# Kernel tuning notes

Hardware: AMD Instinct MI355X
Metric: run time of the kernel (lower is better)

The kernel has to match this reference:

```python
import jax, jax.numpy as jnp
import numpy as np

PAD = 0  # padding_idx for all int feature columns


def setup_inputs() -> dict:
    key = jax.random.key(0)
    ks = jax.random.split(key, 8)
    B = 16384
    return {
        "item_hist": jax.random.randint(ks[0], (B, 50), 0, 100000, dtype=jnp.int64 if jax.config.jax_enable_x64 else jnp.int32).astype(jnp.int32),
        "cate_hist": jax.random.randint(ks[1], (B, 50), 0, 100000).astype(jnp.int32),
        "ctx_ids": jax.random.randint(ks[2], (B, 20), 0, 1000).astype(jnp.int32),
        "price": jax.random.normal(ks[3], (B, 1), dtype=jnp.float32),
        "dense_vec": jax.random.normal(ks[4], (B, 128), dtype=jnp.float32),
        "W_item": jax.random.normal(ks[5], (100000, 64), dtype=jnp.float32),
        "W_cate": jax.random.normal(ks[6], (100000, 64), dtype=jnp.float32),
        "W_ctx": jax.random.normal(ks[7], (1000, 32), dtype=jnp.float32),
    }


def reference(item_hist, cate_hist, ctx_ids, price, dense_vec, W_item, W_cate, W_ctx):
    # torch Embedding with padding_idx: row PAD is zero (and receives no grad)
    Wi = W_item.at[PAD].set(0.0)
    Wc = W_cate.at[PAD].set(0.0)
    Wx = W_ctx.at[PAD].set(0.0)
    # sum merger: [B, L, D] -> [B, D]
    e_item = jnp.take(Wi, item_hist, axis=0).sum(axis=-2)
    # mean merger (divides by L including padding slots, as torch .mean does)
    e_cate = jnp.take(Wc, cate_hist, axis=0).mean(axis=-2)
    # concat merger: [B, L, D] -> [B, L*D]
    B = ctx_ids.shape[0]
    e_ctx = jnp.take(Wx, ctx_ids, axis=0).reshape(B, -1)
    # FeatureLayer concatenates columns in declared order
    return jnp.concatenate([e_item, e_cate, e_ctx, price, dense_vec], axis=-1)
```

## Files before the change

### kernel.cpp

```cpp
#include <hip/hip_runtime.h>


#define LH 50
#define LC 20
#define DI 64
#define DC 64
#define DX 32
#define DDENSE 128
#define OUT_D 897
#define ROWS 4
#define BLK_OUT (ROWS * OUT_D)
#define NROW_TAB 100000
#define TAB_ELEMS (NROW_TAB * 64)
#define NIT8 7

typedef float    f32x4 __attribute__((ext_vector_type(4)));
typedef _Float16 f16x4 __attribute__((ext_vector_type(4)));
typedef _Float16 f16x8 __attribute__((ext_vector_type(8)));

__global__ __launch_bounds__(256) void convert_tables_kernel(
    const float* __restrict__ Wi, const float* __restrict__ Wc,
    _Float16* __restrict__ Hi, _Float16* __restrict__ Hc)
{
    const int stride = gridDim.x * blockDim.x;
    for (int i = blockIdx.x * blockDim.x + threadIdx.x;
         i < TAB_ELEMS / 4; i += stride) {
        const f32x4 a = reinterpret_cast<const f32x4*>(Wi)[i];
        const f32x4 b = reinterpret_cast<const f32x4*>(Wc)[i];
        f16x4 ha, hb;
        #pragma unroll
        for (int e = 0; e < 4; ++e) { ha[e] = (_Float16)a[e]; hb[e] = (_Float16)b[e]; }
        reinterpret_cast<f16x4*>(Hi)[i] = ha;
        reinterpret_cast<f16x4*>(Hc)[i] = hb;
    }
}

template <bool HALF>
__global__ __launch_bounds__(256) void featlayer_kernel(
    const int* __restrict__ item_hist,
    const int* __restrict__ cate_hist,
    const int* __restrict__ ctx_ids,
    const float* __restrict__ price,
    const float* __restrict__ dense_vec,
    const float* __restrict__ W_item,
    const float* __restrict__ W_cate,
    const _Float16* __restrict__ H_item,
    const _Float16* __restrict__ H_cate,
    const float* __restrict__ W_ctx,
    float* __restrict__ out,
    int B)
{
    __shared__ __align__(16) float obuf[BLK_OUT];
    __shared__ int ih_s[ROWS * LH];
    __shared__ int ch_s[ROWS * LH];
    __shared__ int cx_s[ROWS * LC];

    const int t     = threadIdx.x;
    const int rbase = blockIdx.x * ROWS;

    if (t < ROWS * LH) {
        ih_s[t] = item_hist[(size_t)rbase * LH + t];
        ch_s[t] = cate_hist[(size_t)rbase * LH + t];
    }
    if (t < ROWS * LC) cx_s[t] = ctx_ids[(size_t)rbase * LC + t];

    if (t < 128) {
        const int r = t >> 5;
        const int c = t & 31;
        const f32x4 dvv = *reinterpret_cast<const f32x4*>(
            dense_vec + ((size_t)(rbase + r) * DDENSE + c * 4));
        float* o = obuf + r * OUT_D + (DI + DC + LC * DX + 1) + c * 4;
        o[0] = dvv.x; o[1] = dvv.y; o[2] = dvv.z; o[3] = dvv.w;
    }
    if (t < ROWS) obuf[t * OUT_D + DI + DC + LC * DX] = price[rbase + t];

    __syncthreads();

    const int w    = t >> 6;
    const int lane = t & 63;

    if (HALF) {
        const int sub8 = lane >> 3;
        const int l8   = lane & 7;

        int idxI[NIT8], idxC[NIT8];
        #pragma unroll
        for (int k = 0; k < NIT8; ++k) {
            const int ki = sub8 + 8 * k;
            idxI[k] = (ki < LH) ? ih_s[w * LH + ki] : 0;
            idxC[k] = (ki < LH) ? ch_s[w * LH + ki] : 0;
        }

        float iacc[8] = {0,0,0,0,0,0,0,0};
        float cacc[8] = {0,0,0,0,0,0,0,0};
        #pragma unroll
        for (int k = 0; k < NIT8; ++k) {
            const f16x8 vi = *reinterpret_cast<const f16x8*>(
                H_item + ((size_t)idxI[k] * 64 + l8 * 8));
            const f16x8 vc = *reinterpret_cast<const f16x8*>(
                H_cate + ((size_t)idxC[k] * 64 + l8 * 8));
            const float si = (idxI[k] != 0) ? 1.0f : 0.0f;
            const float sc = (idxC[k] != 0) ? 1.0f : 0.0f;
            #pragma unroll
            for (int e = 0; e < 8; ++e) {
                iacc[e] += (float)vi[e] * si;
                cacc[e] += (float)vc[e] * sc;
            }
        }

        #pragma unroll
        for (int e = 0; e < 8; ++e) {
            float a = iacc[e];
            a += __shfl_xor(a, 8, 64);
            a += __shfl_xor(a, 16, 64);
            a += __shfl_xor(a, 32, 64);
            iacc[e] = a;
            float c = cacc[e];
            c += __shfl_xor(c, 8, 64);
            c += __shfl_xor(c, 16, 64);
            c += __shfl_xor(c, 32, 64);
            cacc[e] = c;
        }

        if (sub8 == 0) {
            float* oi = obuf + w * OUT_D + l8 * 8;
            float* oc = obuf + w * OUT_D + DI + l8 * 8;
            const float inv = 1.0f / (float)LH;
            #pragma unroll
            for (int e = 0; e < 8; ++e) {
                oi[e] = iacc[e];
                oc[e] = cacc[e] * inv;
            }
        }
    } else {
        const int sub = lane >> 4;
        const int l16 = lane & 15;
        int idxI[13], idxC[13];
        #pragma unroll
        for (int k = 0; k < 13; ++k) {
            const int ki = sub + 4 * k;
            idxI[k] = (ki < LH) ? ih_s[w * LH + ki] : 0;
            idxC[k] = (ki < LH) ? ch_s[w * LH + ki] : 0;
        }
        f32x4 iacc = {0,0,0,0}, cacc = {0,0,0,0};
        #pragma unroll
        for (int k = 0; k < 13; ++k) {
            const f32x4 vi = *reinterpret_cast<const f32x4*>(
                W_item + ((size_t)idxI[k] * DI + l16 * 4));
            const f32x4 vc = *reinterpret_cast<const f32x4*>(
                W_cate + ((size_t)idxC[k] * DC + l16 * 4));
            iacc += vi * ((idxI[k] != 0) ? 1.0f : 0.0f);
            cacc += vc * ((idxC[k] != 0) ? 1.0f : 0.0f);
        }
        #pragma unroll
        for (int e = 0; e < 4; ++e) {
            float a = iacc[e];
            a += __shfl_xor(a, 16, 64); a += __shfl_xor(a, 32, 64);
            iacc[e] = a;
            float c = cacc[e];
            c += __shfl_xor(c, 16, 64); c += __shfl_xor(c, 32, 64);
            cacc[e] = c;
        }
        if (sub == 0) {
            float* oi = obuf + w * OUT_D + l16 * 4;
            float* oc = obuf + w * OUT_D + DI + l16 * 4;
            const float inv = 1.0f / (float)LH;
            #pragma unroll
            for (int e = 0; e < 4; ++e) { oi[e] = iacc[e]; oc[e] = cacc[e] * inv; }
        }
    }

    #pragma unroll
    for (int t2 = 0; t2 < 3; ++t2) {
        const int c = lane + 64 * t2;
        if (c < (LC * DX) / 4) {
            const int id = cx_s[w * LC + (c >> 3)];
            f32x4 v = {0.f, 0.f, 0.f, 0.f};
            if (id != 0)
                v = *reinterpret_cast<const f32x4*>(
                    W_ctx + ((size_t)id * DX + (c & 7) * 4));
            float* o = obuf + w * OUT_D + DI + DC + 4 * c;
            o[0] = v.x; o[1] = v.y; o[2] = v.z; o[3] = v.w;
        }
    }

    __syncthreads();

    float* __restrict__ oblk = out + (size_t)rbase * OUT_D;
    #pragma unroll
    for (int i = 0; i < 4; ++i) {
        const int c = t + 256 * i;
        if (c < BLK_OUT / 4) {
            const f32x4 v = *reinterpret_cast<const f32x4*>(obuf + 4 * c);
            *reinterpret_cast<f32x4*>(oblk + 4 * c) = v;
        }
    }
}

extern "C" void kernel_launch(void* const* d_in, const int* in_sizes, int n_in,
                              void* d_out, int out_size, void* d_ws, size_t ws_size,
                              hipStream_t stream) {
    const int*   item_hist = (const int*)  d_in[0];
    const int*   cate_hist = (const int*)  d_in[1];
    const int*   ctx_ids   = (const int*)  d_in[2];
    const float* price     = (const float*)d_in[3];
    const float* dense_vec = (const float*)d_in[4];
    const float* W_item    = (const float*)d_in[5];
    const float* W_cate    = (const float*)d_in[6];
    const float* W_ctx     = (const float*)d_in[7];
    float* out = (float*)d_out;

    const int B = in_sizes[0] / LH;
    const int grid = (B + ROWS - 1) / ROWS;

    const size_t tab_bytes = (size_t)TAB_ELEMS * sizeof(_Float16);
    if (ws_size >= 2 * tab_bytes) {
        _Float16* Hi = (_Float16*)d_ws;
        _Float16* Hc = Hi + TAB_ELEMS;
        convert_tables_kernel<<<2048, 256, 0, stream>>>(W_item, W_cate, Hi, Hc);
        featlayer_kernel<true><<<grid, 256, 0, stream>>>(
            item_hist, cate_hist, ctx_ids, price, dense_vec,
            W_item, W_cate, Hi, Hc, W_ctx, out, B);
    } else {
        featlayer_kernel<false><<<grid, 256, 0, stream>>>(
            item_hist, cate_hist, ctx_ids, price, dense_vec,
            W_item, W_cate, nullptr, nullptr, W_ctx, out, B);
    }
}
```

Baseline: 58.36 us.

## Quantize embedding tables to int8 with per-row scales and ctx table to fp16

Replaces the fp16 conversion of the item and category tables with int8 quantization using a per-row absmax scale, and also converts the ctx table to fp16. The gather kernel reads 16 bytes of int8 per lane and dequantizes with the row scale, and the ctx gather reads fp16. This halves conversion writes and gather traffic, at the cost of much larger numerical error from 8-bit quantization.

```diff
diff --git a/kernel.cpp b/kernel.cpp
--- a/kernel.cpp
+++ b/kernel.cpp
@@ -12,30 +12,65 @@
 #define BLK_OUT (ROWS * OUT_D)
 #define NROW_TAB 100000
 #define TAB_ELEMS (NROW_TAB * 64)
-#define NIT8 7
 
 typedef float    f32x4 __attribute__((ext_vector_type(4)));
+typedef int      i32x4 __attribute__((ext_vector_type(4)));
 typedef _Float16 f16x4 __attribute__((ext_vector_type(4)));
 typedef _Float16 f16x8 __attribute__((ext_vector_type(8)));
 
-__global__ __launch_bounds__(256) void convert_tables_kernel(
+#define QI_OFF  0
+#define QC_OFF  6400000
+#define SCI_OFF 12800000
+#define SCC_OFF 13200000
+#define HX_OFF  13600000
+#define WS_NEED 13664000
+#define CONV_TAB_BLOCKS 12500
+#define CTX_CHUNKS 8000
+
+__global__ __launch_bounds__(256) void convert_kernel(
     const float* __restrict__ Wi, const float* __restrict__ Wc,
-    _Float16* __restrict__ Hi, _Float16* __restrict__ Hc)
+    const float* __restrict__ Wx,
+    signed char* __restrict__ Qi, signed char* __restrict__ Qc,
+    float* __restrict__ ScI, float* __restrict__ ScC,
+    _Float16* __restrict__ Hx)
 {
-    const int stride = gridDim.x * blockDim.x;
-    for (int i = blockIdx.x * blockDim.x + threadIdx.x;
-         i < TAB_ELEMS / 4; i += stride) {
-        const f32x4 a = reinterpret_cast<const f32x4*>(Wi)[i];
-        const f32x4 b = reinterpret_cast<const f32x4*>(Wc)[i];
-        f16x4 ha, hb;
-        #pragma unroll
-        for (int e = 0; e < 4; ++e) { ha[e] = (_Float16)a[e]; hb[e] = (_Float16)b[e]; }
-        reinterpret_cast<f16x4*>(Hi)[i] = ha;
-        reinterpret_cast<f16x4*>(Hc)[i] = hb;
+    if (blockIdx.x < CONV_TAB_BLOCKS) {
+        const int gid = blockIdx.x * 256 + threadIdx.x;
+        const int r   = gid >> 4;
+        const int l   = gid & 15;
+        const bool isI = (r < NROW_TAB);
+        const int rr  = isI ? r : r - NROW_TAB;
+        const float* src = (isI ? Wi : Wc) + (size_t)rr * 64;
+        const f32x4 v = *reinterpret_cast<const f32x4*>(src + l * 4);
+        float m = fmaxf(fmaxf(fabsf(v.x), fabsf(v.y)),
+                        fmaxf(fabsf(v.z), fabsf(v.w)));
+        m = fmaxf(m, __shfl_xor(m, 1, 64));
+        m = fmaxf(m, __shfl_xor(m, 2, 64));
+        m = fmaxf(m, __shfl_xor(m, 4, 64));
+        m = fmaxf(m, __shfl_xor(m, 8, 64));
+        const float inv = (m > 0.f) ? 127.0f / m : 0.0f;
+        const int q0 = __float2int_rn(v.x * inv);
+        const int q1 = __float2int_rn(v.y * inv);
+        const int q2 = __float2int_rn(v.z * inv);
+        const int q3 = __float2int_rn(v.w * inv);
+        const unsigned pack = (q0 & 0xff) | ((q1 & 0xff) << 8) |
+                              ((q2 & 0xff) << 16) | ((unsigned)(q3 & 0xff) << 24);
+        signed char* Q = isI ? Qi : Qc;
+        *reinterpret_cast<unsigned*>(Q + (size_t)rr * 64 + l * 4) = pack;
+        if (l == 0) (isI ? ScI : ScC)[rr] = m * (1.0f / 127.0f);
+    } else {
+        const int c = (blockIdx.x - CONV_TAB_BLOCKS) * 256 + threadIdx.x;
+        if (c < CTX_CHUNKS) {
+            const f32x4 v = reinterpret_cast<const f32x4*>(Wx)[c];
+            f16x4 h;
+            #pragma unroll
+            for (int e = 0; e < 4; ++e) h[e] = (_Float16)v[e];
+            reinterpret_cast<f16x4*>(Hx)[c] = h;
+        }
     }
 }
 
-template <bool HALF>
+template <bool QUANT>
 __global__ __launch_bounds__(256) void featlayer_kernel(
     const int* __restrict__ item_hist,
     const int* __restrict__ cate_hist,
@@ -44,8 +79,11 @@
     const float* __restrict__ dense_vec,
     const float* __restrict__ W_item,
     const float* __restrict__ W_cate,
-    const _Float16* __restrict__ H_item,
-    const _Float16* __restrict__ H_cate,
+    const signed char* __restrict__ Qi,
+    const signed char* __restrict__ Qc,
+    const float* __restrict__ ScI,
+    const float* __restrict__ ScC,
+    const _Float16* __restrict__ Hx,
     const float* __restrict__ W_ctx,
     float* __restrict__ out,
     int B)
@@ -79,57 +117,83 @@
     const int w    = t >> 6;
     const int lane = t & 63;
 
-    if (HALF) {
-        const int sub8 = lane >> 3;
-        const int l8   = lane & 7;
-
-        int idxI[NIT8], idxC[NIT8];
-        #pragma unroll
-        for (int k = 0; k < NIT8; ++k) {
-            const int ki = sub8 + 8 * k;
+    if (QUANT) {
+        const int sub16 = lane >> 2;
+        const int l4    = lane & 3;
+
+        int idxI[4], idxC[4];
+        #pragma unroll
+        for (int k = 0; k < 4; ++k) {
+            const int ki = sub16 + 16 * k;
             idxI[k] = (ki < LH) ? ih_s[w * LH + ki] : 0;
             idxC[k] = (ki < LH) ? ch_s[w * LH + ki] : 0;
         }
 
-        float iacc[8] = {0,0,0,0,0,0,0,0};
-        float cacc[8] = {0,0,0,0,0,0,0,0};
-        #pragma unroll
-        for (int k = 0; k < NIT8; ++k) {
-            const f16x8 vi = *reinterpret_cast<const f16x8*>(
-                H_item + ((size_t)idxI[k] * 64 + l8 * 8));
-            const f16x8 vc = *reinterpret_cast<const f16x8*>(
-                H_cate + ((size_t)idxC[k] * 64 + l8 * 8));
-            const float si = (idxI[k] != 0) ? 1.0f : 0.0f;
-            const float sc = (idxC[k] != 0) ? 1.0f : 0.0f;
-            #pragma unroll
-            for (int e = 0; e < 8; ++e) {
-                iacc[e] += (float)vi[e] * si;
-                cacc[e] += (float)vc[e] * sc;
-            }
-        }
-
-        #pragma unroll
-        for (int e = 0; e < 8; ++e) {
+        float iacc[16], cacc[16];
+        #pragma unroll
+        for (int e = 0; e < 16; ++e) { iacc[e] = 0.f; cacc[e] = 0.f; }
+
+        #pragma unroll
+        for (int k = 0; k < 4; ++k) {
+            const i32x4 qi = *reinterpret_cast<const i32x4*>(
+                Qi + ((size_t)idxI[k] * 64 + l4 * 16));
+            const i32x4 qc = *reinterpret_cast<const i32x4*>(
+                Qc + ((size_t)idxC[k] * 64 + l4 * 16));
+            const float fI = (idxI[k] != 0) ? ScI[idxI[k]] : 0.0f;
+            const float fC = (idxC[k] != 0) ? ScC[idxC[k]] : 0.0f;
+            #pragma unroll
+            for (int b = 0; b < 4; ++b) {
+                const int wi = qi[b], wc = qc[b];
+                #pragma unroll
+                for (int j = 0; j < 4; ++j) {
+                    iacc[b * 4 + j] += (float)(signed char)(wi >> (8 * j)) * fI;
+                    cacc[b * 4 + j] += (float)(signed char)(wc >> (8 * j)) * fC;
+                }
+            }
+        }
+
+        #pragma unroll
+        for (int e = 0; e < 16; ++e) {
             float a = iacc[e];
+            a += __shfl_xor(a, 4, 64);
             a += __shfl_xor(a, 8, 64);
             a += __shfl_xor(a, 16, 64);
             a += __shfl_xor(a, 32, 64);
             iacc[e] = a;
             float c = cacc[e];
+            c += __shfl_xor(c, 4, 64);
             c += __shfl_xor(c, 8, 64);
             c += __shfl_xor(c, 16, 64);
             c += __shfl_xor(c, 32, 64);
             cacc[e] = c;
         }
 
-        if (sub8 == 0) {
-            float* oi = obuf + w * OUT_D + l8 * 8;
-            float* oc = obuf + w * OUT_D + DI + l8 * 8;
+        if (sub16 == 0) {
+            float* oi = obuf + w * OUT_D + l4 * 16;
+            float* oc = obuf + w * OUT_D + DI + l4 * 16;
             const float inv = 1.0f / (float)LH;
             #pragma unroll
-            for (int e = 0; e < 8; ++e) {
+            for (int e = 0; e < 16; ++e) {
                 oi[e] = iacc[e];
                 oc[e] = cacc[e] * inv;
+            }
+        }
+
+        #pragma unroll
+        for (int t2 = 0; t2 < 2; ++t2) {
+            const int c = lane + 64 * t2;
+            if (c < (LC * DX) / 8) {
+                const int id = cx_s[w * LC + (c >> 2)];
+                float* o = obuf + w * OUT_D + DI + DC + 8 * c;
+                if (id != 0) {
+                    const f16x8 v = *reinterpret_cast<const f16x8*>(
+                        Hx + ((size_t)id * DX + (c & 3) * 8));
+                    #pragma unroll
+                    for (int e = 0; e < 8; ++e) o[e] = (float)v[e];
+                } else {
+                    #pragma unroll
+                    for (int e = 0; e < 8; ++e) o[e] = 0.0f;
+                }
             }
         }
     } else {
@@ -168,19 +232,18 @@
             #pragma unroll
             for (int e = 0; e < 4; ++e) { oi[e] = iacc[e]; oc[e] = cacc[e] * inv; }
         }
-    }
-
-    #pragma unroll
-    for (int t2 = 0; t2 < 3; ++t2) {
-        const int c = lane + 64 * t2;
-        if (c < (LC * DX) / 4) {
-            const int id = cx_s[w * LC + (c >> 3)];
-            f32x4 v = {0.f, 0.f, 0.f, 0.f};
-            if (id != 0)
-                v = *reinterpret_cast<const f32x4*>(
-                    W_ctx + ((size_t)id * DX + (c & 7) * 4));
-            float* o = obuf + w * OUT_D + DI + DC + 4 * c;
-            o[0] = v.x; o[1] = v.y; o[2] = v.z; o[3] = v.w;
+        #pragma unroll
+        for (int t2 = 0; t2 < 3; ++t2) {
+            const int c = lane + 64 * t2;
+            if (c < (LC * DX) / 4) {
+                const int id = cx_s[w * LC + (c >> 3)];
+                f32x4 v = {0.f, 0.f, 0.f, 0.f};
+                if (id != 0)
+                    v = *reinterpret_cast<const f32x4*>(
+                        W_ctx + ((size_t)id * DX + (c & 7) * 4));
+                float* o = obuf + w * OUT_D + DI + DC + 4 * c;
+                o[0] = v.x; o[1] = v.y; o[2] = v.z; o[3] = v.w;
+            }
         }
     }
 
@@ -213,17 +276,23 @@
     const int B = in_sizes[0] / LH;
     const int grid = (B + ROWS - 1) / ROWS;
 
-    const size_t tab_bytes = (size_t)TAB_ELEMS * sizeof(_Float16);
-    if (ws_size >= 2 * tab_bytes) {
-        _Float16* Hi = (_Float16*)d_ws;
-        _Float16* Hc = Hi + TAB_ELEMS;
-        convert_tables_kernel<<<2048, 256, 0, stream>>>(W_item, W_cate, Hi, Hc);
+    if (ws_size >= WS_NEED) {
+        char* ws = (char*)d_ws;
+        signed char* Qi  = (signed char*)(ws + QI_OFF);
+        signed char* Qc  = (signed char*)(ws + QC_OFF);
+        float*       ScI = (float*)      (ws + SCI_OFF);
+        float*       ScC = (float*)      (ws + SCC_OFF);
+        _Float16*    Hx  = (_Float16*)   (ws + HX_OFF);
+        const int conv_grid = CONV_TAB_BLOCKS + (CTX_CHUNKS + 255) / 256;
+        convert_kernel<<<conv_grid, 256, 0, stream>>>(
+            W_item, W_cate, W_ctx, Qi, Qc, ScI, ScC, Hx);
         featlayer_kernel<true><<<grid, 256, 0, stream>>>(
             item_hist, cate_hist, ctx_ids, price, dense_vec,
-            W_item, W_cate, Hi, Hc, W_ctx, out, B);
+            W_item, W_cate, Qi, Qc, ScI, ScC, Hx, W_ctx, out, B);
     } else {
         featlayer_kernel<false><<<grid, 256, 0, stream>>>(
             item_hist, cate_hist, ctx_ids, price, dense_vec,
-            W_item, W_cate, nullptr, nullptr, W_ctx, out, B);
+            W_item, W_cate, nullptr, nullptr, nullptr, nullptr, nullptr,
+            W_ctx, out, B);
     }
 }
```

New measurement: 61.50 us. +5.4%, slower.
